# Kernel tuning notes

Hardware: AMD Instinct MI355X
Metric: run time of the kernel (lower is better)

Reference implementation:

```python
import jax, jax.numpy as jnp
import numpy as np

NC = 80
NA = 3
NO = NC + 5  # 85
ANCHORS = jnp.array([[[10.,13.],[16.,30.],[33.,23.]],
                     [[30.,61.],[62.,45.],[59.,119.]],
                     [[116.,90.],[156.,198.],[373.,326.]]], dtype=jnp.float32)
STRIDES = (8.0, 16.0, 32.0)
CONF_THRES = 0.25
IOU_THRES = 0.45
NMS_TOPK = 1000   # fixed candidate count for jit-friendly NMS (YOLO caps at max_nms)
MAX_DET = 300
MAX_WH = 4096.0   # class-offset trick from non_max_suppression


def _decode(x, w, b, anchors, stride):
    # x: [B,C,ny,nx]; w: [255,C]; 1x1 conv == channel matmul
    B, _, ny, nx = x.shape
    y = jnp.einsum('bchw,oc->bohw', x, w) + b[None, :, None, None]
    y = y.reshape(B, NA, NO, ny, nx).transpose(0, 1, 3, 4, 2)  # [B,na,ny,nx,no]
    s = jax.nn.sigmoid(y)
    yv, xv = jnp.meshgrid(jnp.arange(ny, dtype=y.dtype), jnp.arange(nx, dtype=y.dtype), indexing='ij')
    grid = jnp.stack((xv, yv), -1) - 0.5                      # [ny,nx,2]
    xy = (s[..., :2] * 2.0 + grid[None, None]) * stride
    wh = (s[..., 2:4] * 2.0) ** 2 * (anchors * stride)[None, :, None, None, :]
    out = jnp.concatenate((xy, wh, s[..., 4:]), axis=-1)
    return out.reshape(B, NA * ny * nx, NO)


def _xywh2xyxy(x):
    xy, wh = x[..., :2], x[..., 2:4]
    return jnp.concatenate([xy - wh * 0.5, xy + wh * 0.5], axis=-1)


def _box_iou(a, b):
    lt = jnp.maximum(a[:, None, :2], b[None, :, :2])
    rb = jnp.minimum(a[:, None, 2:], b[None, :, 2:])
    wh = jnp.clip(rb - lt, 0.0)
    inter = wh[..., 0] * wh[..., 1]
    area_a = (a[:, 2] - a[:, 0]) * (a[:, 3] - a[:, 1])
    area_b = (b[:, 2] - b[:, 0]) * (b[:, 3] - b[:, 1])
    return inter / (area_a[:, None] + area_b[None, :] - inter + 1e-7)


def _nms_single(pred):
    # pred: [N, 85] -> dets [MAX_DET, 6] = (x1,y1,x2,y2,conf,cls), zero-padded
    boxes = _xywh2xyxy(pred[:, :4])
    obj = pred[:, 4]
    cls_conf = pred[:, 5:] * obj[:, None]          # class scores
    score = jnp.max(cls_conf, axis=-1)
    cls = jnp.argmax(cls_conf, axis=-1)
    score = jnp.where(score > CONF_THRES, score, 0.0)
    top_s, idx = jax.lax.top_k(score, NMS_TOPK)    # fixed candidate set
    b = boxes[idx]                                  # [K,4]
    c = cls[idx].astype(b.dtype)
    bo = b + (c * MAX_WH)[:, None]                  # class-aware offset
    iou = _box_iou(bo, bo)                          # [K,K]
    keep0 = top_s > CONF_THRES
    rng = jnp.arange(NMS_TOPK)

    def body(i, keep):
        sup = (iou[i] > IOU_THRES) & (rng > i)
        return jnp.where(keep[i], keep & (~sup), keep)

    keep = jax.lax.fori_loop(0, NMS_TOPK, body, keep0)
    final_s = jnp.where(keep, top_s, 0.0)
    fs, fi = jax.lax.top_k(final_s, MAX_DET)
    det = jnp.concatenate([b[fi], fs[:, None], c[fi][:, None]], axis=-1)  # [MAX_DET,6]
    det = jnp.where((fs > CONF_THRES)[:, None], det, 0.0)
    return det


def setup_inputs() -> dict:
    key = jax.random.key(0)
    ks = jax.random.split(key, 9)
    B = 16
    return {
        'x0': jax.random.normal(ks[0], (B, 128, 80, 80), jnp.float32),
        'x1': jax.random.normal(ks[1], (B, 256, 40, 40), jnp.float32),
        'x2': jax.random.normal(ks[2], (B, 512, 20, 20), jnp.float32),
        'w0': jax.random.normal(ks[3], (255, 128), jnp.float32) * 0.02,
        'b0': jax.random.normal(ks[4], (255,), jnp.float32) * 0.02,
        'w1': jax.random.normal(ks[5], (255, 256), jnp.float32) * 0.02,
        'b1': jax.random.normal(ks[6], (255,), jnp.float32) * 0.02,
        'w2': jax.random.normal(ks[7], (255, 512), jnp.float32) * 0.02,
        'b2': jax.random.normal(ks[8], (255,), jnp.float32) * 0.02,
    }


def reference(x0, x1, x2, w0, b0, w1, b1, w2, b2):
    z0 = _decode(x0, w0, b0, ANCHORS[0], STRIDES[0])
    z1 = _decode(x1, w1, b1, ANCHORS[1], STRIDES[1])
    z2 = _decode(x2, w2, b2, ANCHORS[2], STRIDES[2])
    pred = jnp.concatenate([z0, z1, z2], axis=1)   # [B, 25200, 85]
    dets = jax.vmap(_nms_single)(pred)             # [B, 300, 6]
    return dets, pred
```

## Files before the change

kernel.cpp:

```cpp
#include <hip/hip_runtime.h>
#include <cstdint>

#define BATCH   16
#define NCLS    80
#define NOUT    85
#define NANC    3
#define NCAND   25200
#define CONF    0.25f
#define IOUT    0.45f
#define TOPK    1000
#define MAXDET  300
#define MAXWH   4096.0f
#define CAPK    2048
#define NBH     520
#define XPAD    40

typedef __attribute__((ext_vector_type(8))) short short8;
typedef __attribute__((ext_vector_type(4))) float f32x4;
typedef unsigned int u32;

constexpr size_t SCORE_OFF = 0;
constexpr size_t CLS_OFF   = SCORE_OFF + (size_t)BATCH * NCAND * 4;
constexpr size_t THR_OFF   = CLS_OFF   + (size_t)BATCH * NCAND * 4;
constexpr size_t CNT_OFF   = THR_OFF   + 256;
constexpr size_t KEYS_OFF  = CNT_OFF   + 256;
constexpr size_t RS_OFF    = KEYS_OFF  + (size_t)BATCH * CAPK * 8;
constexpr size_t RBOX_OFF  = RS_OFF    + (size_t)BATCH * TOPK * 4;
constexpr size_t RBO_OFF   = RBOX_OFF  + (size_t)BATCH * TOPK * 16;
constexpr size_t RCLS_OFF  = RBO_OFF   + (size_t)BATCH * TOPK * 16;
constexpr size_t SUP_OFF   = RCLS_OFF  + (size_t)BATCH * TOPK * 4;
constexpr int NL0 = 255 * 128, NL1 = 255 * 256, NL2 = 255 * 512;
constexpr int WB0 = 0, WB1 = 3 * NL0, WB2 = 3 * NL0 + 3 * NL1;

__device__ __forceinline__ ushort bf16rn(float f) {
    uint32_t u = __float_as_uint(f);
    uint32_t r = u + 0x7FFFu + ((u >> 16) & 1u);
    return (ushort)(r >> 16);
}

__device__ __forceinline__ void split3(float v, ushort& s1, ushort& s2, ushort& s3) {
    ushort h1 = bf16rn(v);
    float f1 = __uint_as_float((uint32_t)h1 << 16);
    float r1 = v - f1;
    ushort h2 = bf16rn(r1);
    float f2 = __uint_as_float((uint32_t)h2 << 16);
    ushort h3 = bf16rn(r1 - f2);
    s1 = h1; s2 = h2; s3 = h3;
}

__device__ __forceinline__ void gl_lds16(const float* g, void* l) {
    __builtin_amdgcn_global_load_lds(
        (const __attribute__((address_space(1))) u32*)g,
        (__attribute__((address_space(3))) u32*)l, 16, 0, 0);
}

__global__ __launch_bounds__(256)
void wsplit_kernel(const float* __restrict__ w0, const float* __restrict__ w1,
                   const float* __restrict__ w2, ushort* __restrict__ wsp) {
    int i = blockIdx.x * 256 + threadIdx.x;
    if (i >= NL0 + NL1 + NL2) return;
    const float* src; int idx, base, NL;
    if (i < NL0)            { src = w0; idx = i;             base = WB0; NL = NL0; }
    else if (i < NL0 + NL1) { src = w1; idx = i - NL0;       base = WB1; NL = NL1; }
    else                    { src = w2; idx = i - NL0 - NL1; base = WB2; NL = NL2; }
    ushort s1, s2, s3;
    split3(src[idx], s1, s2, s3);
    wsp[base + idx]          = s1;
    wsp[base + NL + idx]     = s2;
    wsp[base + 2 * NL + idx] = s3;
}

template<int C, int NN>
__device__ __forceinline__ void decode_lds_level(
    const float* __restrict__ xb,
    const ushort* __restrict__ w1p, const ushort* __restrict__ w2p,
    const ushort* __restrict__ w3p, const float* __restrict__ bias,
    float* __restrict__ predB, float* __restrict__ scoreB, int* __restrict__ clsB,
    int tile, int lvlOff, float stride,
    float aw0, float ah0, float aw1, float ah1, float aw2, float ah2,
    char* xsb0, char* xsb1, ushort* x1, ushort* x2, ushort* x3, float* staged)
{
    constexpr int NPOS = NN * NN;
    constexpr int NCHUNK = C / 32;
    constexpr int MAXOFF = C * NPOS - 4;
    const int tid  = threadIdx.x;
    const int lane = tid & 63;
    const int wid  = tid >> 6;
    const int l16  = lane >> 4;
    const int lr   = lane & 15;
    const int pos0 = tile * 64;

    f32x4 acc[4][4];
#pragma unroll
    for (int nf = 0; nf < 4; nf++)
#pragma unroll
        for (int pf = 0; pf < 4; pf++) acc[nf][pf] = (f32x4){0.f, 0.f, 0.f, 0.f};

    const int sp = tid & 63;
    const int wv = tid >> 6;
    char* xsb[2] = {xsb0, xsb1};

#pragma unroll
    for (int i = 0; i < 2; i++) {
        int f = tid + i * 256;
        int kc = f >> 4;
        int p4 = (f & 15) * 4;
        int off = kc * NPOS + pos0 + p4;
        off = off < MAXOFF ? off : MAXOFF;
        gl_lds16(xb + off, xsb[0] + f * 16);
    }

    for (int c = 0; c < NCHUNK; c++) {
        float* xs = (float*)xsb[c & 1];
        __syncthreads();
        if (c + 1 < NCHUNK) {
            const int k0n = (c + 1) * 32;
#pragma unroll
            for (int i = 0; i < 2; i++) {
                int f = tid + i * 256;
                int kc = f >> 4;
                int p4 = (f & 15) * 4;
                int off = (k0n + kc) * NPOS + pos0 + p4;
                off = off < MAXOFF ? off : MAXOFF;
                gl_lds16(xb + off, xsb[(c + 1) & 1] + f * 16);
            }
        }
        {
            short8 s1v, s2v, s3v;
#pragma unroll
            for (int j = 0; j < 8; j++) {
                float f = xs[(wv * 8 + j) * 64 + sp];
                ushort u1, u2, u3;
                split3(f, u1, u2, u3);
                s1v[j] = (short)u1; s2v[j] = (short)u2; s3v[j] = (short)u3;
            }
            int dst = sp * XPAD + ((wv ^ ((sp >> 2) & 3)) << 3);
            *(short8*)(x1 + dst) = s1v;
            *(short8*)(x2 + dst) = s2v;
            *(short8*)(x3 + dst) = s3v;
        }
        asm volatile("s_waitcnt lgkmcnt(0)" ::: "memory");
        __builtin_amdgcn_s_barrier();
        __builtin_amdgcn_sched_barrier(0);
        short8 b1[4], b2[4], b3[4];
#pragma unroll
        for (int pf = 0; pf < 4; pf++) {
            int pr = pf * 16 + lr;
            int off = pr * XPAD + ((l16 ^ (lr >> 2)) << 3);
            b1[pf] = *(const short8*)(x1 + off);
            b2[pf] = *(const short8*)(x2 + off);
            b3[pf] = *(const short8*)(x3 + off);
        }
        const int k0 = c * 32;
#pragma unroll
        for (int nf = 0; nf < 4; nf++) {
            int o = wid * 64 + nf * 16 + lr;
            int oc = o < 255 ? o : 254;
            size_t aoff = (size_t)oc * C + k0 + l16 * 8;
            short8 A1 = *(const short8*)(w1p + aoff);
            short8 A2 = *(const short8*)(w2p + aoff);
            short8 A3 = *(const short8*)(w3p + aoff);
#pragma unroll
            for (int pf = 0; pf < 4; pf++) {
                acc[nf][pf] = __builtin_amdgcn_mfma_f32_16x16x32_bf16(A1, b1[pf], acc[nf][pf], 0, 0, 0);
                acc[nf][pf] = __builtin_amdgcn_mfma_f32_16x16x32_bf16(A1, b2[pf], acc[nf][pf], 0, 0, 0);
                acc[nf][pf] = __builtin_amdgcn_mfma_f32_16x16x32_bf16(A2, b1[pf], acc[nf][pf], 0, 0, 0);
                acc[nf][pf] = __builtin_amdgcn_mfma_f32_16x16x32_bf16(A2, b2[pf], acc[nf][pf], 0, 0, 0);
                acc[nf][pf] = __builtin_amdgcn_mfma_f32_16x16x32_bf16(A1, b3[pf], acc[nf][pf], 0, 0, 0);
                acc[nf][pf] = __builtin_amdgcn_mfma_f32_16x16x32_bf16(A3, b1[pf], acc[nf][pf], 0, 0, 0);
            }
        }
    }

    float bv[16];
#pragma unroll
    for (int nf = 0; nf < 4; nf++)
#pragma unroll
        for (int r = 0; r < 4; r++) {
            int o = wid * 64 + nf * 16 + l16 * 4 + r;
            bv[nf * 4 + r] = (o < 255) ? bias[o] : 0.f;
        }

    const float aw[3] = {aw0, aw1, aw2};
    const float ah[3] = {ah0, ah1, ah2};
    const int validP = (NPOS - pos0) < 64 ? (NPOS - pos0) : 64;

#pragma unroll
    for (int a = 0; a < 3; a++) {
        __syncthreads();
#pragma unroll
        for (int nf = 0; nf < 4; nf++) {
#pragma unroll
            for (int r = 0; r < 4; r++) {
                int o = wid * 64 + nf * 16 + l16 * 4 + r;
                int j = o - a * 85;
                if (o < 255 && j >= 0 && j < 85) {
#pragma unroll
                    for (int pf = 0; pf < 4; pf++) {
                        int p = pf * 16 + lr;
                        int pos = pos0 + p;
                        float y = acc[nf][pf][r] + bv[nf * 4 + r];
                        float s = 1.f / (1.f + __expf(-y));
                        float val;
                        if (j == 0) {
                            int gyi = pos / NN;
                            float gx = (float)(pos - gyi * NN);
                            val = (2.f * s + gx - 0.5f) * stride;
                        } else if (j == 1) {
                            float gy = (float)(pos / NN);
                            val = (2.f * s + gy - 0.5f) * stride;
                        } else if (j == 2) {
                            float t2 = 2.f * s; val = t2 * t2 * aw[a];
                        } else if (j == 3) {
                            float t2 = 2.f * s; val = t2 * t2 * ah[a];
                        } else {
                            val = s;
                        }
                        staged[p * 85 + j] = val;
                    }
                }
            }
        }
        __syncthreads();
        size_t base = ((size_t)lvlOff + (size_t)a * NPOS + pos0) * 85;
        if (validP == 64) {
            const float4* s4 = (const float4*)staged;
            float4* d4 = (float4*)(predB + base);
            for (int q = tid; q < (64 * 85 / 4); q += 256) d4[q] = s4[q];
        } else {
            int tot = validP * 85;
            for (int q = tid; q < tot; q += 256) predB[base + q] = staged[q];
        }
        int p = tid >> 2, c4 = tid & 3;
        if (p < validP) {
            int j0 = 5 + c4 * 20;
            float best = staged[p * 85 + j0];
            int bi = c4 * 20;
#pragma unroll
            for (int jj = 1; jj < 20; jj++) {
                float vv = staged[p * 85 + j0 + jj];
                if (vv > best) { best = vv; bi = c4 * 20 + jj; }
            }
#pragma unroll
            for (int d = 1; d < 4; d <<= 1) {
                float ov = __shfl_xor(best, d);
                int   oi = __shfl_xor(bi, d);
                if (ov > best || (ov == best && oi < bi)) { best = ov; bi = oi; }
            }
            if (c4 == 0) {
                float obj = staged[p * 85 + 4];
                float sc = obj * best;
                int cand = lvlOff + a * NPOS + pos0 + p;
                scoreB[cand] = (sc > CONF) ? sc : 0.f;
                clsB[cand] = bi;
            }
        }
    }
}

__global__ __launch_bounds__(256)
void decode_all_lds_kernel(const float* __restrict__ x0, const float* __restrict__ x1,
                           const float* __restrict__ x2,
                           const float* __restrict__ b0, const float* __restrict__ b1,
                           const float* __restrict__ b2,
                           const ushort* __restrict__ wsp,
                           float* __restrict__ pred,
                           float* __restrict__ scoreArr, int* __restrict__ clsArr)
{
    __shared__ __align__(16) char smem[31744];
    char*   xsb0 = smem;
    char*   xsb1 = smem + 8192;
    ushort* p1   = (ushort*)(smem + 16384);
    ushort* p2   = (ushort*)(smem + 21504);
    ushort* p3   = (ushort*)(smem + 26624);
    float*  staged = (float*)smem;

    const int b = blockIdx.y;
    const int t = blockIdx.x;

    float* predB  = pred + (size_t)b * NCAND * 85;
    float* scoreB = scoreArr + (size_t)b * NCAND;
    int*   clsB   = clsArr + (size_t)b * NCAND;

    if (t < 7) {
        decode_lds_level<512, 20>(x2 + (size_t)b * 512 * 400,
                              wsp + WB2, wsp + WB2 + NL2, wsp + WB2 + 2 * NL2, b2,
                              predB, scoreB, clsB, t, 24000, 32.f,
                              3712.f, 2880.f, 4992.f, 6336.f, 11936.f, 10432.f,
                              xsb0, xsb1, p1, p2, p3, staged);
    } else if (t < 32) {
        decode_lds_level<256, 40>(x1 + (size_t)b * 256 * 1600,
                              wsp + WB1, wsp + WB1 + NL1, wsp + WB1 + 2 * NL1, b1,
                              predB, scoreB, clsB, t - 7, 19200, 16.f,
                              480.f, 976.f, 992.f, 720.f, 944.f, 1904.f,
                              xsb0, xsb1, p1, p2, p3, staged);
    } else {
        decode_lds_level<128, 80>(x0 + (size_t)b * 128 * 6400,
                              wsp + WB0, wsp + WB0 + NL0, wsp + WB0 + 2 * NL0, b0,
                              predB, scoreB, clsB, t - 32, 0, 8.f,
                              80.f, 104.f, 128.f, 240.f, 264.f, 184.f,
                              xsb0, xsb1, p1, p2, p3, staged);
    }
}

__global__ __launch_bounds__(1024)
void select1_kernel(const float* __restrict__ score, const float* __restrict__ pred,
                    const int* __restrict__ clsArr, int* __restrict__ nArr,
                    float* __restrict__ rs, float* __restrict__ rbox,
                    float* __restrict__ rbo, float* __restrict__ rcls) {
    int img = blockIdx.x, tid = threadIdx.x;
    __shared__ uint64_t sk[CAPK];
    __shared__ uint32_t h[NBH];
    __shared__ uint32_t sfx[1024 + 1];
    __shared__ int bucketSh;
    __shared__ uint32_t cntS;
    for (int i = tid; i < NBH; i += 1024) h[i] = 0;
    for (int i = tid; i < CAPK; i += 1024) sk[i] = 0ull;
    if (tid == 0) cntS = 0u;
    __syncthreads();
    const float* s = score + (size_t)img * NCAND;
    for (int i = tid; i < NCAND; i += 1024) {
        float v = s[i];
        if (v > CONF) {
            int bk = (int)((__float_as_uint(v) >> 15) - 0x7D00u);
            bk = bk < 0 ? 0 : (bk >= NBH ? NBH - 1 : bk);
            atomicAdd(&h[bk], 1u);
        }
    }
    __syncthreads();
    sfx[tid] = (tid < NBH) ? h[tid] : 0u;
    if (tid == 0) sfx[1024] = 0u;
    __syncthreads();
    for (int off = 1; off < 1024; off <<= 1) {
        uint32_t v = sfx[tid] + ((tid + off < 1024) ? sfx[tid + off] : 0u);
        __syncthreads();
        sfx[tid] = v;
        __syncthreads();
    }
    uint32_t M = sfx[0];
    uint32_t target = M < TOPK ? M : TOPK;
    if (M > 0 && tid < NBH && sfx[tid] >= target && sfx[tid + 1] < target)
        bucketSh = tid;
    __syncthreads();
    uint32_t thr = (M == 0) ? 0xFFFFFFFFu : ((uint32_t)(bucketSh + 0x7D00) << 15);
    for (int i = tid; i < NCAND; i += 1024) {
        float v = s[i];
        if (v > CONF) {
            uint32_t bits = __float_as_uint(v);
            if (bits >= thr) {
                uint32_t pos = atomicAdd(&cntS, 1u);
                if (pos < CAPK)
                    sk[pos] = ((uint64_t)bits << 32) | (uint32_t)(~(uint32_t)i);
            }
        }
    }
    __syncthreads();
    uint32_t n = cntS < CAPK ? cntS : CAPK;
    for (int k = 2; k <= CAPK; k <<= 1)
        for (int j = k >> 1; j > 0; j >>= 1) {
            for (int i = tid; i < CAPK; i += 1024) {
                int l = i ^ j;
                if (l > i) {
                    uint64_t a = sk[i], b = sk[l];
                    bool descRegion = ((i & k) == 0);
                    bool sw = descRegion ? (a < b) : (a > b);
                    if (sw) { sk[i] = b; sk[l] = a; }
                }
            }
            __syncthreads();
        }
    for (int r = tid; r < TOPK; r += 1024) {
        float sc = 0.f; uint32_t idx = 0;
        if (r < (int)n) {
            uint64_t key = sk[r];
            sc = __uint_as_float((uint32_t)(key >> 32));
            idx = ~(uint32_t)key;
        }
        const float* pr = pred + ((size_t)img * NCAND + idx) * 85;
        float cx = pr[0], cy = pr[1], ww = pr[2], hh = pr[3];
        float x1 = cx - ww * 0.5f, y1 = cy - hh * 0.5f;
        float x2 = cx + ww * 0.5f, y2 = cy + hh * 0.5f;
        float c = (float)clsArr[(size_t)img * NCAND + idx];
        float off = c * MAXWH;
        size_t rb = ((size_t)img * TOPK + r) * 4;
        rbox[rb + 0] = x1; rbox[rb + 1] = y1; rbox[rb + 2] = x2; rbox[rb + 3] = y2;
        rbo[rb + 0] = x1 + off; rbo[rb + 1] = y1 + off;
        rbo[rb + 2] = x2 + off; rbo[rb + 3] = y2 + off;
        rs[(size_t)img * TOPK + r] = sc;
        rcls[(size_t)img * TOPK + r] = c;
    }
    if (tid == 0) nArr[img] = (int)(n < TOPK ? n : TOPK);
}

__global__ __launch_bounds__(256)
void sup_kernel(const float* __restrict__ rbo, uint64_t* __restrict__ sup) {
    int img = blockIdx.y;
    int wid = threadIdx.x >> 6, lane = threadIdx.x & 63;
    int i = blockIdx.x * 4 + wid;
    if (i >= TOPK) return;
    const float* bi_ = rbo + ((size_t)img * TOPK + i) * 4;
    float ax1 = bi_[0], ay1 = bi_[1], ax2 = bi_[2], ay2 = bi_[3];
    float areaA = (ax2 - ax1) * (ay2 - ay1);
    for (int w = 0; w < 16; w++) {
        int j = w * 64 + lane;
        bool cond = false;
        if (j < TOPK && j > i) {
            const float* bj = rbo + ((size_t)img * TOPK + j) * 4;
            float bx1 = bj[0], by1 = bj[1], bx2 = bj[2], by2 = bj[3];
            float ltx = fmaxf(ax1, bx1), lty = fmaxf(ay1, by1);
            float rbx = fminf(ax2, bx2), rby = fminf(ay2, by2);
            float iw = fmaxf(rbx - ltx, 0.f), ih = fmaxf(rby - lty, 0.f);
            float inter = iw * ih;
            float areaB = (bx2 - bx1) * (by2 - by1);
            float iou = inter / (areaA + areaB - inter + 1e-7f);
            cond = iou > IOUT;
        }
        unsigned long long m = __ballot(cond);
        if (lane == w) sup[(((size_t)img * TOPK) + i) * 16 + w] = m;
    }
}

__global__ __launch_bounds__(64)
void greedy_final_kernel(const int* __restrict__ nArr, const uint64_t* __restrict__ sup,
                         const float* __restrict__ rbox, const float* __restrict__ rs,
                         const float* __restrict__ rcls, float* __restrict__ dets) {
    int img = blockIdx.x, lane = threadIdx.x;
    __shared__ uint32_t keep32[32];
    __shared__ uint16_t accList[64];
    __shared__ int ordL[MAXDET];
    int nkeep = nArr[img];
    for (int w = 0; w < 16; w++) {
        int r = w * 64 + lane;
        bool k = (r < TOPK) && (r < nkeep);
        unsigned long long m = __ballot(k);
        if (lane == 0) {
            keep32[2 * w]     = (uint32_t)m;
            keep32[2 * w + 1] = (uint32_t)(m >> 32);
        }
    }
    __syncthreads();
    const uint64_t* supim = sup + (size_t)img * TOPK * 16;
    int kept = 0;
    for (int wb = 0; wb < 16 && kept < MAXDET; wb++) {
        uint64_t word = ((uint64_t)keep32[2 * wb + 1] << 32) | keep32[2 * wb];
        if (!word) continue;
        uint64_t diag = 0;
        int myIdx = wb * 64 + lane;
        if (myIdx < TOPK) diag = supim[(size_t)myIdx * 16 + wb];
        uint64_t cur = word, acc = 0;
        for (int b = 0; b < 64; b++) {
            uint64_t row = __shfl(diag, b);
            if ((cur >> b) & 1ull) { acc |= 1ull << b; cur &= ~row; }
            if (!cur) break;
        }
        int nb = __popcll(acc);
        if (kept + nb > MAXDET) {
            int t = MAXDET - kept;
            bool mine = (acc >> lane) & 1ull;
            int rank = __popcll(acc & ((1ull << lane) - 1ull));
            acc = __ballot(mine && rank < t);
            nb = t;
        }
        {
            bool mine = (acc >> lane) & 1ull;
            int rank = __popcll(acc & ((1ull << lane) - 1ull));
            if (mine) {
                ordL[kept + rank] = wb * 64 + lane;
                accList[rank] = (uint16_t)(wb * 64 + lane);
            }
        }
        kept += nb;
        if (kept >= MAXDET) break;
        __syncthreads();
        int nw = 15 - wb;
        if (nw > 0 && nb > 0) {
            int P = nb * nw;
            for (int p = lane; p < P; p += 64) {
                int bi = p / nw, wq = wb + 1 + p % nw;
                int srcIdx = accList[bi];
                uint64_t row = supim[(size_t)srcIdx * 16 + wq];
                uint32_t lo = (uint32_t)row, hi = (uint32_t)(row >> 32);
                if (lo) atomicAnd(&keep32[2 * wq], ~lo);
                if (hi) atomicAnd(&keep32[2 * wq + 1], ~hi);
            }
        }
        __syncthreads();
    }
    __syncthreads();
    float* d = dets + (size_t)img * MAXDET * 6;
    for (int q = lane; q < MAXDET * 6; q += 64) d[q] = 0.f;
    __syncthreads();
    for (int r = lane; r < kept; r += 64) {
        int i = ordL[r];
        const float* bx = rbox + ((size_t)img * TOPK + i) * 4;
        d[r * 6 + 0] = bx[0]; d[r * 6 + 1] = bx[1];
        d[r * 6 + 2] = bx[2]; d[r * 6 + 3] = bx[3];
        d[r * 6 + 4] = rs[(size_t)img * TOPK + i];
        d[r * 6 + 5] = rcls[(size_t)img * TOPK + i];
    }
}

extern "C" void kernel_launch(void* const* d_in, const int* in_sizes, int n_in,
                              void* d_out, int out_size, void* d_ws, size_t ws_size,
                              hipStream_t stream) {
    const float* x0 = (const float*)d_in[0];
    const float* x1 = (const float*)d_in[1];
    const float* x2 = (const float*)d_in[2];
    const float* w0 = (const float*)d_in[3];
    const float* b0 = (const float*)d_in[4];
    const float* w1 = (const float*)d_in[5];
    const float* b1 = (const float*)d_in[6];
    const float* w2 = (const float*)d_in[7];
    const float* b2 = (const float*)d_in[8];

    float* dets = (float*)d_out;
    float* pred = dets + (size_t)BATCH * MAXDET * 6;

    char* ws = (char*)d_ws;
    float*    scoreArr = (float*)   (ws + SCORE_OFF);
    int*      clsArr   = (int*)     (ws + CLS_OFF);
    int*      nArr     = (int*)     (ws + THR_OFF);
    float*    rs       = (float*)   (ws + RS_OFF);
    float*    rbox     = (float*)   (ws + RBOX_OFF);
    float*    rbo      = (float*)   (ws + RBO_OFF);
    float*    rcls     = (float*)   (ws + RCLS_OFF);
    uint64_t* sup      = (uint64_t*)(ws + SUP_OFF);
    ushort*   wsp      = (ushort*)  (ws + SUP_OFF);

    wsplit_kernel<<<(NL0 + NL1 + NL2 + 255) / 256, 256, 0, stream>>>(w0, w1, w2, wsp);

    decode_all_lds_kernel<<<dim3(132, BATCH), 256, 0, stream>>>(
        x0, x1, x2, b0, b1, b2, wsp, pred, scoreArr, clsArr);

    select1_kernel<<<BATCH, 1024, 0, stream>>>(scoreArr, pred, clsArr, nArr,
                                               rs, rbox, rbo, rcls);
    sup_kernel<<<dim3(250, BATCH), 256, 0, stream>>>(rbo, sup);
    greedy_final_kernel<<<BATCH, 64, 0, stream>>>(nArr, sup, rbox, rs, rcls, dets);
}
```

Before: 261.8 us.

## Triple-buffer activation loads and prefetch weight fragments before the MFMA loop

Turns the double-buffered global-to-LDS activation pipeline into a three-stage ring with a prefetch distance of two chunks. It waits on vmcnt(2) with a raw barrier instead of using __syncthreads. Weight fragments for all four output tiles are now loaded at the top of each chunk, so their latency overlaps the split/convert work. This costs 8 KB more LDS per block and extra registers, which may reduce occupancy, and it issues redundant dummy loads past the last chunk.

```diff
diff --git a/kernel.cpp b/kernel.cpp
--- a/kernel.cpp
+++ b/kernel.cpp
@@ -78,7 +78,8 @@
     float* __restrict__ predB, float* __restrict__ scoreB, int* __restrict__ clsB,
     int tile, int lvlOff, float stride,
     float aw0, float ah0, float aw1, float ah1, float aw2, float ah2,
-    char* xsb0, char* xsb1, ushort* x1, ushort* x2, ushort* x3, float* staged)
+    char* xsb0, char* xsb1, char* xsb2,
+    ushort* x1, ushort* x2, ushort* x3, float* staged)
 {
     constexpr int NPOS = NN * NN;
     constexpr int NCHUNK = C / 32;
@@ -98,33 +99,58 @@
 
     const int sp = tid & 63;
     const int wv = tid >> 6;
-    char* xsb[2] = {xsb0, xsb1};
-
-#pragma unroll
-    for (int i = 0; i < 2; i++) {
-        int f = tid + i * 256;
+    char* xsb[3] = {xsb0, xsb1, xsb2};
+
+#pragma unroll
+    for (int s = 0; s < 2; s++) {
+        int f = tid;
         int kc = f >> 4;
         int p4 = (f & 15) * 4;
-        int off = kc * NPOS + pos0 + p4;
-        off = off < MAXOFF ? off : MAXOFF;
-        gl_lds16(xb + off, xsb[0] + f * 16);
+#pragma unroll
+        for (int i = 0; i < 2; i++) {
+            int ff = f + i * 256;
+            int kcc = ff >> 4;
+            int pp4 = (ff & 15) * 4;
+            int off = (s * 32 + kcc) * NPOS + pos0 + pp4;
+            off = off < MAXOFF ? off : MAXOFF;
+            gl_lds16(xb + off, xsb[s] + ff * 16);
+        }
+        (void)kc; (void)p4;
     }
 
     for (int c = 0; c < NCHUNK; c++) {
-        float* xs = (float*)xsb[c & 1];
-        __syncthreads();
-        if (c + 1 < NCHUNK) {
-            const int k0n = (c + 1) * 32;
+        float* xs = (float*)xsb[c % 3];
+        asm volatile("s_waitcnt vmcnt(2) lgkmcnt(0)" ::: "memory");
+        __builtin_amdgcn_s_barrier();
+        __builtin_amdgcn_sched_barrier(0);
+        short8 A1v[4], A2v[4], A3v[4];
+        {
+            const int k0 = c * 32;
+#pragma unroll
+            for (int nf = 0; nf < 4; nf++) {
+                int o = wid * 64 + nf * 16 + lr;
+                int oc = o < 255 ? o : 254;
+                size_t aoff = (size_t)oc * C + k0 + l16 * 8;
+                A1v[nf] = *(const short8*)(w1p + aoff);
+                A2v[nf] = *(const short8*)(w2p + aoff);
+                A3v[nf] = *(const short8*)(w3p + aoff);
+            }
+        }
+        __builtin_amdgcn_sched_barrier(0);
+        {
+            const int cr = (c + 2 < NCHUNK) ? (c + 2) : 0;
+            char* dst = xsb[(c + 2) % 3];
 #pragma unroll
             for (int i = 0; i < 2; i++) {
                 int f = tid + i * 256;
                 int kc = f >> 4;
                 int p4 = (f & 15) * 4;
-                int off = (k0n + kc) * NPOS + pos0 + p4;
+                int off = (cr * 32 + kc) * NPOS + pos0 + p4;
                 off = off < MAXOFF ? off : MAXOFF;
-                gl_lds16(xb + off, xsb[(c + 1) & 1] + f * 16);
-            }
-        }
+                gl_lds16(xb + off, dst + f * 16);
+            }
+        }
+        __builtin_amdgcn_sched_barrier(0);
         {
             short8 s1v, s2v, s3v;
 #pragma unroll
@@ -151,23 +177,16 @@
             b2[pf] = *(const short8*)(x2 + off);
             b3[pf] = *(const short8*)(x3 + off);
         }
-        const int k0 = c * 32;
 #pragma unroll
         for (int nf = 0; nf < 4; nf++) {
-            int o = wid * 64 + nf * 16 + lr;
-            int oc = o < 255 ? o : 254;
-            size_t aoff = (size_t)oc * C + k0 + l16 * 8;
-            short8 A1 = *(const short8*)(w1p + aoff);
-            short8 A2 = *(const short8*)(w2p + aoff);
-            short8 A3 = *(const short8*)(w3p + aoff);
 #pragma unroll
             for (int pf = 0; pf < 4; pf++) {
-                acc[nf][pf] = __builtin_amdgcn_mfma_f32_16x16x32_bf16(A1, b1[pf], acc[nf][pf], 0, 0, 0);
-                acc[nf][pf] = __builtin_amdgcn_mfma_f32_16x16x32_bf16(A1, b2[pf], acc[nf][pf], 0, 0, 0);
-                acc[nf][pf] = __builtin_amdgcn_mfma_f32_16x16x32_bf16(A2, b1[pf], acc[nf][pf], 0, 0, 0);
-                acc[nf][pf] = __builtin_amdgcn_mfma_f32_16x16x32_bf16(A2, b2[pf], acc[nf][pf], 0, 0, 0);
-                acc[nf][pf] = __builtin_amdgcn_mfma_f32_16x16x32_bf16(A1, b3[pf], acc[nf][pf], 0, 0, 0);
-                acc[nf][pf] = __builtin_amdgcn_mfma_f32_16x16x32_bf16(A3, b1[pf], acc[nf][pf], 0, 0, 0);
+                acc[nf][pf] = __builtin_amdgcn_mfma_f32_16x16x32_bf16(A1v[nf], b1[pf], acc[nf][pf], 0, 0, 0);
+                acc[nf][pf] = __builtin_amdgcn_mfma_f32_16x16x32_bf16(A1v[nf], b2[pf], acc[nf][pf], 0, 0, 0);
+                acc[nf][pf] = __builtin_amdgcn_mfma_f32_16x16x32_bf16(A2v[nf], b1[pf], acc[nf][pf], 0, 0, 0);
+                acc[nf][pf] = __builtin_amdgcn_mfma_f32_16x16x32_bf16(A2v[nf], b2[pf], acc[nf][pf], 0, 0, 0);
+                acc[nf][pf] = __builtin_amdgcn_mfma_f32_16x16x32_bf16(A1v[nf], b3[pf], acc[nf][pf], 0, 0, 0);
+                acc[nf][pf] = __builtin_amdgcn_mfma_f32_16x16x32_bf16(A3v[nf], b1[pf], acc[nf][pf], 0, 0, 0);
             }
         }
     }
@@ -267,12 +286,13 @@
                            float* __restrict__ pred,
                            float* __restrict__ scoreArr, int* __restrict__ clsArr)
 {
-    __shared__ __align__(16) char smem[31744];
+    __shared__ __align__(16) char smem[39936];
     char*   xsb0 = smem;
     char*   xsb1 = smem + 8192;
-    ushort* p1   = (ushort*)(smem + 16384);
-    ushort* p2   = (ushort*)(smem + 21504);
-    ushort* p3   = (ushort*)(smem + 26624);
+    char*   xsb2 = smem + 16384;
+    ushort* p1   = (ushort*)(smem + 24576);
+    ushort* p2   = (ushort*)(smem + 29696);
+    ushort* p3   = (ushort*)(smem + 34816);
     float*  staged = (float*)smem;
 
     const int b = blockIdx.y;
@@ -287,19 +307,19 @@
                               wsp + WB2, wsp + WB2 + NL2, wsp + WB2 + 2 * NL2, b2,
                               predB, scoreB, clsB, t, 24000, 32.f,
                               3712.f, 2880.f, 4992.f, 6336.f, 11936.f, 10432.f,
-                              xsb0, xsb1, p1, p2, p3, staged);
+                              xsb0, xsb1, xsb2, p1, p2, p3, staged);
     } else if (t < 32) {
         decode_lds_level<256, 40>(x1 + (size_t)b * 256 * 1600,
                               wsp + WB1, wsp + WB1 + NL1, wsp + WB1 + 2 * NL1, b1,
                               predB, scoreB, clsB, t - 7, 19200, 16.f,
                               480.f, 976.f, 992.f, 720.f, 944.f, 1904.f,
-                              xsb0, xsb1, p1, p2, p3, staged);
+                              xsb0, xsb1, xsb2, p1, p2, p3, staged);
     } else {
         decode_lds_level<128, 80>(x0 + (size_t)b * 128 * 6400,
                               wsp + WB0, wsp + WB0 + NL0, wsp + WB0 + 2 * NL0, b0,
                               predB, scoreB, clsB, t - 32, 0, 8.f,
                               80.f, 104.f, 128.f, 240.f, 264.f, 184.f,
-                              xsb0, xsb1, p1, p2, p3, staged);
+                              xsb0, xsb1, xsb2, p1, p2, p3, staged);
     }
 }
 
```

Measured after the change: 265.8 us. Within noise of the previous version (+1.5%).

## Replace three-way bf16 split GEMM with scaled two-way fp16 split

Applied to the files above, without the earlier changes.

The 1x1-conv matmul emulated fp32 with a three-term bf16 split and six MFMAs per fragment. It now uses a two-term fp16 split with the residual scaled by 2048, accumulated into separate main and correction accumulators, for three MFMAs per fragment. This halves the split work and the LDS and weight traffic and shrinks shared memory. The cost is more accumulator registers and lower precision, since fp16 has a narrow exponent range and could overflow or underflow on unusual inputs.

```diff
diff --git a/kernel.cpp b/kernel.cpp
--- a/kernel.cpp
+++ b/kernel.cpp
@@ -14,8 +14,9 @@
 #define CAPK    2048
 #define NBH     520
 #define XPAD    40
-
-typedef __attribute__((ext_vector_type(8))) short short8;
+#define CSCALE  2048.0f
+
+typedef __attribute__((ext_vector_type(8))) _Float16 half8;
 typedef __attribute__((ext_vector_type(4))) float f32x4;
 typedef unsigned int u32;
 
@@ -30,22 +31,13 @@
 constexpr size_t RCLS_OFF  = RBO_OFF   + (size_t)BATCH * TOPK * 16;
 constexpr size_t SUP_OFF   = RCLS_OFF  + (size_t)BATCH * TOPK * 4;
 constexpr int NL0 = 255 * 128, NL1 = 255 * 256, NL2 = 255 * 512;
-constexpr int WB0 = 0, WB1 = 3 * NL0, WB2 = 3 * NL0 + 3 * NL1;
-
-__device__ __forceinline__ ushort bf16rn(float f) {
-    uint32_t u = __float_as_uint(f);
-    uint32_t r = u + 0x7FFFu + ((u >> 16) & 1u);
-    return (ushort)(r >> 16);
-}
-
-__device__ __forceinline__ void split3(float v, ushort& s1, ushort& s2, ushort& s3) {
-    ushort h1 = bf16rn(v);
-    float f1 = __uint_as_float((uint32_t)h1 << 16);
-    float r1 = v - f1;
-    ushort h2 = bf16rn(r1);
-    float f2 = __uint_as_float((uint32_t)h2 << 16);
-    ushort h3 = bf16rn(r1 - f2);
-    s1 = h1; s2 = h2; s3 = h3;
+constexpr int WB0 = 0, WB1 = 2 * NL0, WB2 = 2 * NL0 + 2 * NL1;
+
+__device__ __forceinline__ void split2h(float v, _Float16& h1, _Float16& h2) {
+    _Float16 a = (_Float16)v;
+    float af = (float)a;
+    _Float16 b = (_Float16)((v - af) * CSCALE);
+    h1 = a; h2 = b;
 }
 
 __device__ __forceinline__ void gl_lds16(const float* g, void* l) {
@@ -63,22 +55,22 @@
     if (i < NL0)            { src = w0; idx = i;             base = WB0; NL = NL0; }
     else if (i < NL0 + NL1) { src = w1; idx = i - NL0;       base = WB1; NL = NL1; }
     else                    { src = w2; idx = i - NL0 - NL1; base = WB2; NL = NL2; }
-    ushort s1, s2, s3;
-    split3(src[idx], s1, s2, s3);
-    wsp[base + idx]          = s1;
-    wsp[base + NL + idx]     = s2;
-    wsp[base + 2 * NL + idx] = s3;
+    _Float16 h1, h2;
+    split2h(src[idx], h1, h2);
+    _Float16* p = (_Float16*)wsp;
+    p[base + idx]      = h1;
+    p[base + NL + idx] = h2;
 }
 
 template<int C, int NN>
 __device__ __forceinline__ void decode_lds_level(
     const float* __restrict__ xb,
     const ushort* __restrict__ w1p, const ushort* __restrict__ w2p,
-    const ushort* __restrict__ w3p, const float* __restrict__ bias,
+    const float* __restrict__ bias,
     float* __restrict__ predB, float* __restrict__ scoreB, int* __restrict__ clsB,
     int tile, int lvlOff, float stride,
     float aw0, float ah0, float aw1, float ah1, float aw2, float ah2,
-    char* xsb0, char* xsb1, ushort* x1, ushort* x2, ushort* x3, float* staged)
+    char* xsb0, char* xsb1, ushort* x1, ushort* x2, float* staged)
 {
     constexpr int NPOS = NN * NN;
     constexpr int NCHUNK = C / 32;
@@ -90,11 +82,14 @@
     const int lr   = lane & 15;
     const int pos0 = tile * 64;
 
-    f32x4 acc[4][4];
+    f32x4 accM[4][4], accC[4][4];
 #pragma unroll
     for (int nf = 0; nf < 4; nf++)
 #pragma unroll
-        for (int pf = 0; pf < 4; pf++) acc[nf][pf] = (f32x4){0.f, 0.f, 0.f, 0.f};
+        for (int pf = 0; pf < 4; pf++) {
+            accM[nf][pf] = (f32x4){0.f, 0.f, 0.f, 0.f};
+            accC[nf][pf] = (f32x4){0.f, 0.f, 0.f, 0.f};
+        }
 
     const int sp = tid & 63;
     const int wv = tid >> 6;
@@ -126,30 +121,28 @@
             }
         }
         {
-            short8 s1v, s2v, s3v;
+            half8 s1v, s2v;
 #pragma unroll
             for (int j = 0; j < 8; j++) {
                 float f = xs[(wv * 8 + j) * 64 + sp];
-                ushort u1, u2, u3;
-                split3(f, u1, u2, u3);
-                s1v[j] = (short)u1; s2v[j] = (short)u2; s3v[j] = (short)u3;
+                _Float16 u1, u2;
+                split2h(f, u1, u2);
+                s1v[j] = u1; s2v[j] = u2;
             }
             int dst = sp * XPAD + ((wv ^ ((sp >> 2) & 3)) << 3);
-            *(short8*)(x1 + dst) = s1v;
-            *(short8*)(x2 + dst) = s2v;
-            *(short8*)(x3 + dst) = s3v;
+            *(half8*)(x1 + dst) = s1v;
+            *(half8*)(x2 + dst) = s2v;
         }
         asm volatile("s_waitcnt lgkmcnt(0)" ::: "memory");
         __builtin_amdgcn_s_barrier();
         __builtin_amdgcn_sched_barrier(0);
-        short8 b1[4], b2[4], b3[4];
+        half8 b1[4], b2[4];
 #pragma unroll
         for (int pf = 0; pf < 4; pf++) {
             int pr = pf * 16 + lr;
             int off = pr * XPAD + ((l16 ^ (lr >> 2)) << 3);
-            b1[pf] = *(const short8*)(x1 + off);
-            b2[pf] = *(const short8*)(x2 + off);
-            b3[pf] = *(const short8*)(x3 + off);
+            b1[pf] = *(const half8*)(x1 + off);
+            b2[pf] = *(const half8*)(x2 + off);
         }
         const int k0 = c * 32;
 #pragma unroll
@@ -157,17 +150,13 @@
             int o = wid * 64 + nf * 16 + lr;
             int oc = o < 255 ? o : 254;
             size_t aoff = (size_t)oc * C + k0 + l16 * 8;
-            short8 A1 = *(const short8*)(w1p + aoff);
-            short8 A2 = *(const short8*)(w2p + aoff);
-            short8 A3 = *(const short8*)(w3p + aoff);
+            half8 A1 = *(const half8*)(w1p + aoff);
+            half8 A2 = *(const half8*)(w2p + aoff);
 #pragma unroll
             for (int pf = 0; pf < 4; pf++) {
-                acc[nf][pf] = __builtin_amdgcn_mfma_f32_16x16x32_bf16(A1, b1[pf], acc[nf][pf], 0, 0, 0);
-                acc[nf][pf] = __builtin_amdgcn_mfma_f32_16x16x32_bf16(A1, b2[pf], acc[nf][pf], 0, 0, 0);
-                acc[nf][pf] = __builtin_amdgcn_mfma_f32_16x16x32_bf16(A2, b1[pf], acc[nf][pf], 0, 0, 0);
-                acc[nf][pf] = __builtin_amdgcn_mfma_f32_16x16x32_bf16(A2, b2[pf], acc[nf][pf], 0, 0, 0);
-                acc[nf][pf] = __builtin_amdgcn_mfma_f32_16x16x32_bf16(A1, b3[pf], acc[nf][pf], 0, 0, 0);
-                acc[nf][pf] = __builtin_amdgcn_mfma_f32_16x16x32_bf16(A3, b1[pf], acc[nf][pf], 0, 0, 0);
+                accM[nf][pf] = __builtin_amdgcn_mfma_f32_16x16x32_f16(A1, b1[pf], accM[nf][pf], 0, 0, 0);
+                accC[nf][pf] = __builtin_amdgcn_mfma_f32_16x16x32_f16(A1, b2[pf], accC[nf][pf], 0, 0, 0);
+                accC[nf][pf] = __builtin_amdgcn_mfma_f32_16x16x32_f16(A2, b1[pf], accC[nf][pf], 0, 0, 0);
             }
         }
     }
@@ -184,6 +173,7 @@
     const float aw[3] = {aw0, aw1, aw2};
     const float ah[3] = {ah0, ah1, ah2};
     const int validP = (NPOS - pos0) < 64 ? (NPOS - pos0) : 64;
+    const float inv = 1.0f / CSCALE;
 
 #pragma unroll
     for (int a = 0; a < 3; a++) {
@@ -199,7 +189,7 @@
                     for (int pf = 0; pf < 4; pf++) {
                         int p = pf * 16 + lr;
                         int pos = pos0 + p;
-                        float y = acc[nf][pf][r] + bv[nf * 4 + r];
+                        float y = fmaf(accC[nf][pf][r], inv, accM[nf][pf][r]) + bv[nf * 4 + r];
                         float s = 1.f / (1.f + __expf(-y));
                         float val;
                         if (j == 0) {
@@ -267,12 +257,11 @@
                            float* __restrict__ pred,
                            float* __restrict__ scoreArr, int* __restrict__ clsArr)
 {
-    __shared__ __align__(16) char smem[31744];
+    __shared__ __align__(16) char smem[26624];
     char*   xsb0 = smem;
     char*   xsb1 = smem + 8192;
     ushort* p1   = (ushort*)(smem + 16384);
     ushort* p2   = (ushort*)(smem + 21504);
-    ushort* p3   = (ushort*)(smem + 26624);
     float*  staged = (float*)smem;
 
     const int b = blockIdx.y;
@@ -284,22 +273,22 @@
 
     if (t < 7) {
         decode_lds_level<512, 20>(x2 + (size_t)b * 512 * 400,
-                              wsp + WB2, wsp + WB2 + NL2, wsp + WB2 + 2 * NL2, b2,
+                              wsp + WB2, wsp + WB2 + NL2, b2,
                               predB, scoreB, clsB, t, 24000, 32.f,
                               3712.f, 2880.f, 4992.f, 6336.f, 11936.f, 10432.f,
-                              xsb0, xsb1, p1, p2, p3, staged);
+                              xsb0, xsb1, p1, p2, staged);
     } else if (t < 32) {
         decode_lds_level<256, 40>(x1 + (size_t)b * 256 * 1600,
-                              wsp + WB1, wsp + WB1 + NL1, wsp + WB1 + 2 * NL1, b1,
+                              wsp + WB1, wsp + WB1 + NL1, b1,
                               predB, scoreB, clsB, t - 7, 19200, 16.f,
                               480.f, 976.f, 992.f, 720.f, 944.f, 1904.f,
-                              xsb0, xsb1, p1, p2, p3, staged);
+                              xsb0, xsb1, p1, p2, staged);
     } else {
         decode_lds_level<128, 80>(x0 + (size_t)b * 128 * 6400,
-                              wsp + WB0, wsp + WB0 + NL0, wsp + WB0 + 2 * NL0, b0,
+                              wsp + WB0, wsp + WB0 + NL0, b0,
                               predB, scoreB, clsB, t - 32, 0, 8.f,
                               80.f, 104.f, 128.f, 240.f, 264.f, 184.f,
-                              xsb0, xsb1, p1, p2, p3, staged);
+                              xsb0, xsb1, p1, p2, staged);
     }
 }
 
```

New measurement: 288.5 us. 1.1x slower.
